# Kernel optimization log

Measured on AMD Instinct MI355X. Metric: run time of the kernel, lower is better.

## Reference

```python
import jax, jax.numpy as jnp
import numpy as np

TOPK = 2
NUM_BODY_POINTS = 17
HIDDEN = 64


def bilinear_grid_sample(feat, grid):
    """F.grid_sample(feat, grid, mode='bilinear', padding_mode='zeros', align_corners=False).
    feat: [B,C,H,W]; grid: [B,L,K,2] in [-1,1], grid[...,0]=x (width), grid[...,1]=y (height).
    Returns [B,C,L,K]."""
    B, C, H, W = feat.shape
    x = (grid[..., 0] + 1.0) * (0.5 * W) - 0.5  # [B,L,K]
    y = (grid[..., 1] + 1.0) * (0.5 * H) - 0.5
    x0 = jnp.floor(x)
    y0 = jnp.floor(y)
    wx1 = x - x0
    wy1 = y - y0
    featf = feat.reshape(B, C, H * W)

    def gather(xi, yi):
        valid = (xi >= 0) & (xi < W) & (yi >= 0) & (yi < H)  # [B,L,K]
        xc = jnp.clip(xi, 0, W - 1).astype(jnp.int32)
        yc = jnp.clip(yi, 0, H - 1).astype(jnp.int32)
        idx = (yc * W + xc).reshape(B, -1)  # [B, L*K]
        v = jax.vmap(lambda f, i: f[:, i])(featf, idx)  # [B,C,L*K]
        v = v.reshape(B, C, *xi.shape[1:])  # [B,C,L,K]
        return v * valid[:, None].astype(feat.dtype)

    w00 = ((1 - wx1) * (1 - wy1))[:, None]
    w10 = (wx1 * (1 - wy1))[:, None]
    w01 = ((1 - wx1) * wy1)[:, None]
    w11 = (wx1 * wy1)[:, None]
    return (gather(x0, y0) * w00 + gather(x0 + 1, y0) * w10
            + gather(x0, y0 + 1) * w01 + gather(x0 + 1, y0 + 1) * w11)


def setup_inputs() -> dict:
    key = jax.random.key(0)
    ks = jax.random.split(key, 8)
    B, L, K, C, H, Wd = 16, 1000, NUM_BODY_POINTS, 17, 256, 256
    in_dim = K * (TOPK + 1)
    scores = jax.random.normal(ks[0], (B, L, 1), dtype=jnp.float32)
    pred_poses = jax.random.uniform(ks[1], (B, L, 2 * K), dtype=jnp.float32)
    feat = jax.random.normal(ks[2], (B, C, H, Wd), dtype=jnp.float32)
    s1 = 1.0 / np.sqrt(in_dim)
    s2 = 1.0 / np.sqrt(HIDDEN)
    w1 = jax.random.uniform(ks[3], (HIDDEN, in_dim), minval=-s1, maxval=s1, dtype=jnp.float32)
    b1 = jax.random.uniform(ks[4], (HIDDEN,), minval=-s1, maxval=s1, dtype=jnp.float32)
    w2 = jax.random.uniform(ks[5], (1, HIDDEN), minval=-s2, maxval=s2, dtype=jnp.float32)
    b2 = jax.random.uniform(ks[6], (1,), minval=-s2, maxval=s2, dtype=jnp.float32)
    return {"scores": scores, "pred_poses": pred_poses, "feat": feat,
            "w1": w1, "b1": b1, "w2": w2, "b2": b2}


def reference(scores, pred_poses, feat, w1, b1, w2, b2):
    B, L = pred_poses.shape[:2]
    poses = pred_poses.reshape(B, L, NUM_BODY_POINTS, 2)
    sampled = bilinear_grid_sample(feat, 2.0 * poses - 1.0)  # [B,C,L,K]
    sampled = jnp.transpose(sampled, (0, 2, 3, 1))  # [B,L,K,C]
    prob_topk, _ = jax.lax.top_k(sampled, TOPK)  # [B,L,K,topk]
    stat = jnp.concatenate([prob_topk, prob_topk.mean(axis=-1, keepdims=True)], axis=-1)
    x = stat.reshape(B, L, -1)  # [B,L,K*(topk+1)]
    h = jax.nn.relu(jnp.einsum('bli,hi->blh', x, w1) + b1)
    quality = jnp.einsum('blh,oh->blo', h, w2) + b2  # [B,L,1]
    return scores + quality
```

## Files before the change

kernel.cpp:

```cpp
#include <hip/hip_runtime.h>
#include <hip/hip_bf16.h>
#include <math.h>

#define NB 16
#define NL 1000
#define NK 17
#define NC 17
#define NH 256
#define NW 256
#define HID 64
#define IN_DIM 51
#define PPB 15
#define NPAIR (NB*NL)
#define PADC 20
#define PAIRS_PER_XCD 2000
#define BLKS_PER_XCD 134

#define TOP2(v) do { const float _v = (v); \
    if (_v > m1) { m2 = m1; m1 = _v; } else if (_v > m2) { m2 = _v; } } while (0)

__global__ __launch_bounds__(256) void transpose_feat(
    const float* __restrict__ feat, float* __restrict__ featT)
{
    __shared__ float s[NC][257];
    const int bid = blockIdx.x;
    const int l   = ((bid & 7) << 9) | (bid >> 3);
    const int b   = l >> 8;
    const int hw0 = (l & 255) << 8;
    const int tid = threadIdx.x;
    const float* fb = feat + (size_t)b * NC * (NH * NW) + hw0;
    #pragma unroll
    for (int c = 0; c < NC; ++c)
        s[c][tid] = fb[c * (NH * NW) + tid];
    __syncthreads();
    float4* outp = reinterpret_cast<float4*>(
        featT + ((size_t)b * (NH * NW) + hw0) * PADC);
    #pragma unroll
    for (int i = tid; i < 256 * PADC / 4; i += 256) {
        const int p = i / 5;
        const int j = i - 5 * p;
        float4 v;
        if (j < 4) {
            const int c = 4 * j;
            v = make_float4(s[c][p], s[c + 1][p], s[c + 2][p], s[c + 3][p]);
        } else {
            v = make_float4(s[16][p], 0.f, 0.f, 0.f);
        }
        outp[i] = v;
    }
}

__global__ __launch_bounds__(256) void lqe_fused_t(
    const float* __restrict__ scores,
    const float* __restrict__ pred_poses,
    const float* __restrict__ featT,
    const float* __restrict__ w1,
    const float* __restrict__ b1,
    const float* __restrict__ w2,
    const float* __restrict__ b2,
    float* __restrict__ out)
{
    __shared__ float s_w1[HID * IN_DIM];
    __shared__ float s_b1[HID];
    __shared__ float s_w2[HID];
    __shared__ float s_x[PPB][IN_DIM + 1];

    const int tid = threadIdx.x;
    const int xcd    = blockIdx.x & 7;
    const int idx    = blockIdx.x >> 3;
    const int local0 = idx * PPB;

    for (int i = tid; i < HID * IN_DIM; i += 256) s_w1[i] = w1[i];
    if (tid < HID) { s_b1[tid] = b1[tid]; s_w2[tid] = w2[tid]; }

    if (tid < PPB * NK) {
        const int lp = tid / NK;
        const int k  = tid - lp * NK;
        const int local = local0 + lp;
        if (local < PAIRS_PER_XCD) {
            const int pair = xcd * PAIRS_PER_XCD + local;
            const int b = pair / NL;
            const float2 p = *reinterpret_cast<const float2*>(
                pred_poses + (size_t)pair * (2 * NK) + 2 * k);
            const float gx = 2.0f * p.x - 1.0f;
            const float gy = 2.0f * p.y - 1.0f;
            const float fx = (gx + 1.0f) * (0.5f * NW) - 0.5f;
            const float fy = (gy + 1.0f) * (0.5f * NH) - 0.5f;
            const float x0f = floorf(fx), y0f = floorf(fy);
            const float wx = fx - x0f,   wy = fy - y0f;
            const int ix0 = (int)x0f, iy0 = (int)y0f;
            const int ix1 = ix0 + 1,  iy1 = iy0 + 1;
            const float vx0 = (ix0 >= 0 && ix0 < NW) ? 1.f : 0.f;
            const float vx1 = (ix1 >= 0 && ix1 < NW) ? 1.f : 0.f;
            const float vy0 = (iy0 >= 0 && iy0 < NH) ? 1.f : 0.f;
            const float vy1 = (iy1 >= 0 && iy1 < NH) ? 1.f : 0.f;
            const float w00 = (1.f - wx) * (1.f - wy) * vx0 * vy0;
            const float w10 = wx * (1.f - wy) * vx1 * vy0;
            const float w01 = (1.f - wx) * wy * vx0 * vy1;
            const float w11 = wx * wy * vx1 * vy1;
            const int cx0 = min(max(ix0, 0), NW - 1), cx1 = min(max(ix1, 0), NW - 1);
            const int cy0 = min(max(iy0, 0), NH - 1), cy1 = min(max(iy1, 0), NH - 1);
            const float* fb = featT + (size_t)b * (NH * NW) * PADC;
            const float* p00 = fb + (size_t)(cy0 * NW + cx0) * PADC;
            const float* p10 = fb + (size_t)(cy0 * NW + cx1) * PADC;
            const float* p01 = fb + (size_t)(cy1 * NW + cx0) * PADC;
            const float* p11 = fb + (size_t)(cy1 * NW + cx1) * PADC;

            float m1 = -INFINITY, m2 = -INFINITY;
            #pragma unroll
            for (int j = 0; j < 4; ++j) {
                const float4 a = *reinterpret_cast<const float4*>(p00 + 4 * j);
                const float4 bq = *reinterpret_cast<const float4*>(p10 + 4 * j);
                const float4 c = *reinterpret_cast<const float4*>(p01 + 4 * j);
                const float4 d = *reinterpret_cast<const float4*>(p11 + 4 * j);
                TOP2(w00 * a.x + w10 * bq.x + w01 * c.x + w11 * d.x);
                TOP2(w00 * a.y + w10 * bq.y + w01 * c.y + w11 * d.y);
                TOP2(w00 * a.z + w10 * bq.z + w01 * c.z + w11 * d.z);
                TOP2(w00 * a.w + w10 * bq.w + w01 * c.w + w11 * d.w);
            }
            TOP2(w00 * p00[16] + w10 * p10[16] + w01 * p01[16] + w11 * p11[16]);

            s_x[lp][3 * k + 0] = m1;
            s_x[lp][3 * k + 1] = m2;
            s_x[lp][3 * k + 2] = 0.5f * (m1 + m2);
        }
    }
    __syncthreads();

    const int wv = tid >> 6;
    const int lane = tid & 63;
    const float vb2 = b2[0];
    for (int lp = wv; lp < PPB; lp += 4) {
        if (local0 + lp >= PAIRS_PER_XCD) break;
        const int pair = xcd * PAIRS_PER_XCD + local0 + lp;
        float h = s_b1[lane];
        #pragma unroll
        for (int i = 0; i < IN_DIM; ++i)
            h = fmaf(s_x[lp][i], s_w1[lane * IN_DIM + i], h);
        h = fmaxf(h, 0.f);
        float pval = h * s_w2[lane];
        #pragma unroll
        for (int off = 32; off >= 1; off >>= 1)
            pval += __shfl_xor(pval, off, 64);
        if (lane == 0) out[pair] = scores[pair] + pval + vb2;
    }
}

__global__ __launch_bounds__(256) void lqe_fused_direct(
    const float* __restrict__ scores,
    const float* __restrict__ pred_poses,
    const float* __restrict__ feat,
    const float* __restrict__ w1,
    const float* __restrict__ b1,
    const float* __restrict__ w2,
    const float* __restrict__ b2,
    float* __restrict__ out)
{
    __shared__ float s_w1[HID * IN_DIM];
    __shared__ float s_b1[HID];
    __shared__ float s_w2[HID];
    __shared__ float s_x[PPB][IN_DIM + 1];

    const int tid = threadIdx.x;
    for (int i = tid; i < HID * IN_DIM; i += 256) s_w1[i] = w1[i];
    if (tid < HID) { s_b1[tid] = b1[tid]; s_w2[tid] = w2[tid]; }

    if (tid < PPB * NK) {
        const int lp = tid / NK;
        const int k  = tid - lp * NK;
        const int pair = blockIdx.x * PPB + lp;
        if (pair < NPAIR) {
            const int b = pair / NL;
            const float2 p = *reinterpret_cast<const float2*>(
                pred_poses + (size_t)pair * (2 * NK) + 2 * k);
            const float gx = 2.0f * p.x - 1.0f;
            const float gy = 2.0f * p.y - 1.0f;
            const float fx = (gx + 1.0f) * (0.5f * NW) - 0.5f;
            const float fy = (gy + 1.0f) * (0.5f * NH) - 0.5f;
            const float x0f = floorf(fx), y0f = floorf(fy);
            const float wx = fx - x0f,   wy = fy - y0f;
            const int ix0 = (int)x0f, iy0 = (int)y0f;
            const int ix1 = ix0 + 1,  iy1 = iy0 + 1;
            const float vx0 = (ix0 >= 0 && ix0 < NW) ? 1.f : 0.f;
            const float vx1 = (ix1 >= 0 && ix1 < NW) ? 1.f : 0.f;
            const float vy0 = (iy0 >= 0 && iy0 < NH) ? 1.f : 0.f;
            const float vy1 = (iy1 >= 0 && iy1 < NH) ? 1.f : 0.f;
            const float w00 = (1.f - wx) * (1.f - wy) * vx0 * vy0;
            const float w10 = wx * (1.f - wy) * vx1 * vy0;
            const float w01 = (1.f - wx) * wy * vx0 * vy1;
            const float w11 = wx * wy * vx1 * vy1;
            const int cx0 = min(max(ix0, 0), NW - 1), cx1 = min(max(ix1, 0), NW - 1);
            const int cy0 = min(max(iy0, 0), NH - 1), cy1 = min(max(iy1, 0), NH - 1);
            const int o00 = cy0 * NW + cx0, o10 = cy0 * NW + cx1;
            const int o01 = cy1 * NW + cx0, o11 = cy1 * NW + cx1;
            const float* fb = feat + (size_t)b * NC * NH * NW;
            float m1 = -INFINITY, m2 = -INFINITY;
            #pragma unroll
            for (int c = 0; c < NC; ++c) {
                const float* fc = fb + c * (NH * NW);
                TOP2(w00 * fc[o00] + w10 * fc[o10] + w01 * fc[o01] + w11 * fc[o11]);
            }
            s_x[lp][3 * k + 0] = m1;
            s_x[lp][3 * k + 1] = m2;
            s_x[lp][3 * k + 2] = 0.5f * (m1 + m2);
        }
    }
    __syncthreads();

    const int wv = tid >> 6;
    const int lane = tid & 63;
    const float vb2 = b2[0];
    for (int lp = wv; lp < PPB; lp += 4) {
        const int pair = blockIdx.x * PPB + lp;
        if (pair >= NPAIR) break;
        float h = s_b1[lane];
        #pragma unroll
        for (int i = 0; i < IN_DIM; ++i)
            h = fmaf(s_x[lp][i], s_w1[lane * IN_DIM + i], h);
        h = fmaxf(h, 0.f);
        float pval = h * s_w2[lane];
        #pragma unroll
        for (int off = 32; off >= 1; off >>= 1)
            pval += __shfl_xor(pval, off, 64);
        if (lane == 0) out[pair] = scores[pair] + pval + vb2;
    }
}

extern "C" void kernel_launch(void* const* d_in, const int* in_sizes, int n_in,
                              void* d_out, int out_size, void* d_ws, size_t ws_size,
                              hipStream_t stream) {
    const float* scores     = (const float*)d_in[0];
    const float* pred_poses = (const float*)d_in[1];
    const float* feat       = (const float*)d_in[2];
    const float* w1         = (const float*)d_in[3];
    const float* b1         = (const float*)d_in[4];
    const float* w2         = (const float*)d_in[5];
    const float* b2         = (const float*)d_in[6];
    float* out = (float*)d_out;

    const size_t needT = (size_t)NB * NH * NW * PADC * sizeof(float);

    if (ws_size >= needT) {
        float* featT = (float*)d_ws;
        transpose_feat<<<NB * 256, 256, 0, stream>>>(feat, featT);
        lqe_fused_t<<<8 * BLKS_PER_XCD, 256, 0, stream>>>(
            scores, pred_poses, featT, w1, b1, w2, b2, out);
    } else {
        const int grid = (NPAIR + PPB - 1) / PPB;
        lqe_fused_direct<<<grid, 256, 0, stream>>>(scores, pred_poses, feat,
                                                   w1, b1, w2, b2, out);
    }
}
```

Before: 163.6 us.

## Split fused sampling/MLP kernel into per-sample gather and register-weight MLP kernels

Replaces the fused sample+MLP kernel with two kernels: one thread per (pair, keypoint) sample computes bilinear top-2 stats and writes them to a workspace buffer, and a separate MLP kernel keeps each lane's w1 row in registers and processes 32 pairs per block. This aims to use all threads during the gather and to stop reloading weights into shared memory alongside the gather phase. It adds an extra launch and a global round trip for the stat buffer, and requires more workspace.

```diff
diff --git a/kernel.cpp b/kernel.cpp
--- a/kernel.cpp
+++ b/kernel.cpp
@@ -10,11 +10,14 @@
 #define NW 256
 #define HID 64
 #define IN_DIM 51
-#define PPB 15
 #define NPAIR (NB*NL)
 #define PADC 20
-#define PAIRS_PER_XCD 2000
-#define BLKS_PER_XCD 134
+#define STATW 52
+#define NSAMP (NPAIR*NK)
+#define SAMP_PER_XCD (NSAMP/8)
+#define BLKS_B 133
+#define PPB_C 32
+#define PPB_F 15
 
 #define TOP2(v) do { const float _v = (v); \
     if (_v > m1) { m2 = m1; m1 = _v; } else if (_v > m2) { m2 = _v; } } while (0)
@@ -50,10 +53,69 @@
     }
 }
 
-__global__ __launch_bounds__(256) void lqe_fused_t(
-    const float* __restrict__ scores,
+__global__ __launch_bounds__(256) void sample_top2(
     const float* __restrict__ pred_poses,
     const float* __restrict__ featT,
+    float* __restrict__ stat)
+{
+    const int xcd = blockIdx.x & 7;
+    const int idx = blockIdx.x >> 3;
+    const int sl  = idx * 256 + threadIdx.x;
+    if (sl >= SAMP_PER_XCD) return;
+    const int s    = xcd * SAMP_PER_XCD + sl;
+    const int pair = s / NK;
+    const int k    = s - pair * NK;
+    const int b    = pair / NL;
+
+    const float2 p = *reinterpret_cast<const float2*>(
+        pred_poses + (size_t)pair * (2 * NK) + 2 * k);
+    const float gx = 2.0f * p.x - 1.0f;
+    const float gy = 2.0f * p.y - 1.0f;
+    const float fx = (gx + 1.0f) * (0.5f * NW) - 0.5f;
+    const float fy = (gy + 1.0f) * (0.5f * NH) - 0.5f;
+    const float x0f = floorf(fx), y0f = floorf(fy);
+    const float wx = fx - x0f,   wy = fy - y0f;
+    const int ix0 = (int)x0f, iy0 = (int)y0f;
+    const int ix1 = ix0 + 1,  iy1 = iy0 + 1;
+    const float vx0 = (ix0 >= 0 && ix0 < NW) ? 1.f : 0.f;
+    const float vx1 = (ix1 >= 0 && ix1 < NW) ? 1.f : 0.f;
+    const float vy0 = (iy0 >= 0 && iy0 < NH) ? 1.f : 0.f;
+    const float vy1 = (iy1 >= 0 && iy1 < NH) ? 1.f : 0.f;
+    const float w00 = (1.f - wx) * (1.f - wy) * vx0 * vy0;
+    const float w10 = wx * (1.f - wy) * vx1 * vy0;
+    const float w01 = (1.f - wx) * wy * vx0 * vy1;
+    const float w11 = wx * wy * vx1 * vy1;
+    const int cx0 = min(max(ix0, 0), NW - 1), cx1 = min(max(ix1, 0), NW - 1);
+    const int cy0 = min(max(iy0, 0), NH - 1), cy1 = min(max(iy1, 0), NH - 1);
+    const float* fb  = featT + (size_t)b * (NH * NW) * PADC;
+    const float* p00 = fb + (size_t)(cy0 * NW + cx0) * PADC;
+    const float* p10 = fb + (size_t)(cy0 * NW + cx1) * PADC;
+    const float* p01 = fb + (size_t)(cy1 * NW + cx0) * PADC;
+    const float* p11 = fb + (size_t)(cy1 * NW + cx1) * PADC;
+
+    float m1 = -INFINITY, m2 = -INFINITY;
+    #pragma unroll
+    for (int j = 0; j < 4; ++j) {
+        const float4 a  = *reinterpret_cast<const float4*>(p00 + 4 * j);
+        const float4 bq = *reinterpret_cast<const float4*>(p10 + 4 * j);
+        const float4 c  = *reinterpret_cast<const float4*>(p01 + 4 * j);
+        const float4 d  = *reinterpret_cast<const float4*>(p11 + 4 * j);
+        TOP2(w00 * a.x + w10 * bq.x + w01 * c.x + w11 * d.x);
+        TOP2(w00 * a.y + w10 * bq.y + w01 * c.y + w11 * d.y);
+        TOP2(w00 * a.z + w10 * bq.z + w01 * c.z + w11 * d.z);
+        TOP2(w00 * a.w + w10 * bq.w + w01 * c.w + w11 * d.w);
+    }
+    TOP2(w00 * p00[16] + w10 * p10[16] + w01 * p01[16] + w11 * p11[16]);
+
+    float* sp = stat + (size_t)pair * STATW + 3 * k;
+    sp[0] = m1;
+    sp[1] = m2;
+    sp[2] = 0.5f * (m1 + m2);
+}
+
+__global__ __launch_bounds__(256) void mlp_head(
+    const float* __restrict__ scores,
+    const float* __restrict__ stat,
     const float* __restrict__ w1,
     const float* __restrict__ b1,
     const float* __restrict__ w2,
@@ -63,82 +125,31 @@
     __shared__ float s_w1[HID * IN_DIM];
     __shared__ float s_b1[HID];
     __shared__ float s_w2[HID];
-    __shared__ float s_x[PPB][IN_DIM + 1];
-
     const int tid = threadIdx.x;
-    const int xcd    = blockIdx.x & 7;
-    const int idx    = blockIdx.x >> 3;
-    const int local0 = idx * PPB;
-
     for (int i = tid; i < HID * IN_DIM; i += 256) s_w1[i] = w1[i];
     if (tid < HID) { s_b1[tid] = b1[tid]; s_w2[tid] = w2[tid]; }
-
-    if (tid < PPB * NK) {
-        const int lp = tid / NK;
-        const int k  = tid - lp * NK;
-        const int local = local0 + lp;
-        if (local < PAIRS_PER_XCD) {
-            const int pair = xcd * PAIRS_PER_XCD + local;
-            const int b = pair / NL;
-            const float2 p = *reinterpret_cast<const float2*>(
-                pred_poses + (size_t)pair * (2 * NK) + 2 * k);
-            const float gx = 2.0f * p.x - 1.0f;
-            const float gy = 2.0f * p.y - 1.0f;
-            const float fx = (gx + 1.0f) * (0.5f * NW) - 0.5f;
-            const float fy = (gy + 1.0f) * (0.5f * NH) - 0.5f;
-            const float x0f = floorf(fx), y0f = floorf(fy);
-            const float wx = fx - x0f,   wy = fy - y0f;
-            const int ix0 = (int)x0f, iy0 = (int)y0f;
-            const int ix1 = ix0 + 1,  iy1 = iy0 + 1;
-            const float vx0 = (ix0 >= 0 && ix0 < NW) ? 1.f : 0.f;
-            const float vx1 = (ix1 >= 0 && ix1 < NW) ? 1.f : 0.f;
-            const float vy0 = (iy0 >= 0 && iy0 < NH) ? 1.f : 0.f;
-            const float vy1 = (iy1 >= 0 && iy1 < NH) ? 1.f : 0.f;
-            const float w00 = (1.f - wx) * (1.f - wy) * vx0 * vy0;
-            const float w10 = wx * (1.f - wy) * vx1 * vy0;
-            const float w01 = (1.f - wx) * wy * vx0 * vy1;
-            const float w11 = wx * wy * vx1 * vy1;
-            const int cx0 = min(max(ix0, 0), NW - 1), cx1 = min(max(ix1, 0), NW - 1);
-            const int cy0 = min(max(iy0, 0), NH - 1), cy1 = min(max(iy1, 0), NH - 1);
-            const float* fb = featT + (size_t)b * (NH * NW) * PADC;
-            const float* p00 = fb + (size_t)(cy0 * NW + cx0) * PADC;
-            const float* p10 = fb + (size_t)(cy0 * NW + cx1) * PADC;
-            const float* p01 = fb + (size_t)(cy1 * NW + cx0) * PADC;
-            const float* p11 = fb + (size_t)(cy1 * NW + cx1) * PADC;
-
-            float m1 = -INFINITY, m2 = -INFINITY;
-            #pragma unroll
-            for (int j = 0; j < 4; ++j) {
-                const float4 a = *reinterpret_cast<const float4*>(p00 + 4 * j);
-                const float4 bq = *reinterpret_cast<const float4*>(p10 + 4 * j);
-                const float4 c = *reinterpret_cast<const float4*>(p01 + 4 * j);
-                const float4 d = *reinterpret_cast<const float4*>(p11 + 4 * j);
-                TOP2(w00 * a.x + w10 * bq.x + w01 * c.x + w11 * d.x);
-                TOP2(w00 * a.y + w10 * bq.y + w01 * c.y + w11 * d.y);
-                TOP2(w00 * a.z + w10 * bq.z + w01 * c.z + w11 * d.z);
-                TOP2(w00 * a.w + w10 * bq.w + w01 * c.w + w11 * d.w);
-            }
-            TOP2(w00 * p00[16] + w10 * p10[16] + w01 * p01[16] + w11 * p11[16]);
-
-            s_x[lp][3 * k + 0] = m1;
-            s_x[lp][3 * k + 1] = m2;
-            s_x[lp][3 * k + 2] = 0.5f * (m1 + m2);
-        }
-    }
     __syncthreads();
 
-    const int wv = tid >> 6;
     const int lane = tid & 63;
+    const int wv   = tid >> 6;
+    float w1r[IN_DIM];
+    #pragma unroll
+    for (int i = 0; i < IN_DIM; ++i) w1r[i] = s_w1[lane * IN_DIM + i];
+    const float hb = s_b1[lane];
+    const float hw = s_w2[lane];
     const float vb2 = b2[0];
-    for (int lp = wv; lp < PPB; lp += 4) {
-        if (local0 + lp >= PAIRS_PER_XCD) break;
-        const int pair = xcd * PAIRS_PER_XCD + local0 + lp;
-        float h = s_b1[lane];
+
+    const int p0 = blockIdx.x * PPB_C + wv * (PPB_C / 4);
+    #pragma unroll
+    for (int j = 0; j < PPB_C / 4; ++j) {
+        const int pair = p0 + j;
+        const float* xp = stat + (size_t)pair * STATW;
+        float h = hb;
         #pragma unroll
         for (int i = 0; i < IN_DIM; ++i)
-            h = fmaf(s_x[lp][i], s_w1[lane * IN_DIM + i], h);
+            h = fmaf(xp[i], w1r[i], h);
         h = fmaxf(h, 0.f);
-        float pval = h * s_w2[lane];
+        float pval = h * hw;
         #pragma unroll
         for (int off = 32; off >= 1; off >>= 1)
             pval += __shfl_xor(pval, off, 64);
@@ -159,16 +170,16 @@
     __shared__ float s_w1[HID * IN_DIM];
     __shared__ float s_b1[HID];
     __shared__ float s_w2[HID];
-    __shared__ float s_x[PPB][IN_DIM + 1];
+    __shared__ float s_x[PPB_F][IN_DIM + 1];
 
     const int tid = threadIdx.x;
     for (int i = tid; i < HID * IN_DIM; i += 256) s_w1[i] = w1[i];
     if (tid < HID) { s_b1[tid] = b1[tid]; s_w2[tid] = w2[tid]; }
 
-    if (tid < PPB * NK) {
+    if (tid < PPB_F * NK) {
         const int lp = tid / NK;
         const int k  = tid - lp * NK;
-        const int pair = blockIdx.x * PPB + lp;
+        const int pair = blockIdx.x * PPB_F + lp;
         if (pair < NPAIR) {
             const int b = pair / NL;
             const float2 p = *reinterpret_cast<const float2*>(
@@ -210,8 +221,8 @@
     const int wv = tid >> 6;
     const int lane = tid & 63;
     const float vb2 = b2[0];
-    for (int lp = wv; lp < PPB; lp += 4) {
-        const int pair = blockIdx.x * PPB + lp;
+    for (int lp = wv; lp < PPB_F; lp += 4) {
+        const int pair = blockIdx.x * PPB_F + lp;
         if (pair >= NPAIR) break;
         float h = s_b1[lane];
         #pragma unroll
@@ -238,15 +249,18 @@
     const float* b2         = (const float*)d_in[6];
     float* out = (float*)d_out;
 
-    const size_t needT = (size_t)NB * NH * NW * PADC * sizeof(float);
-
-    if (ws_size >= needT) {
+    const size_t bytesT = (size_t)NB * NH * NW * PADC * sizeof(float);
+    const size_t bytesS = (size_t)NPAIR * STATW * sizeof(float);
+
+    if (ws_size >= bytesT + bytesS) {
         float* featT = (float*)d_ws;
+        float* stat  = (float*)((char*)d_ws + bytesT);
         transpose_feat<<<NB * 256, 256, 0, stream>>>(feat, featT);
-        lqe_fused_t<<<8 * BLKS_PER_XCD, 256, 0, stream>>>(
-            scores, pred_poses, featT, w1, b1, w2, b2, out);
+        sample_top2<<<8 * BLKS_B, 256, 0, stream>>>(pred_poses, featT, stat);
+        mlp_head<<<NPAIR / PPB_C, 256, 0, stream>>>(scores, stat,
+                                                    w1, b1, w2, b2, out);
     } else {
-        const int grid = (NPAIR + PPB - 1) / PPB;
+        const int grid = (NPAIR + PPB_F - 1) / PPB_F;
         lqe_fused_direct<<<grid, 256, 0, stream>>>(scores, pred_poses, feat,
                                                    w1, b1, w2, b2, out);
     }
```

After: 179.2 us. +9.5%, slower.
